# Performance work log

Hardware: AMD Instinct MI355X
Metric: run time of the kernel (lower is better)

Reference implementation:

```python
import jax, jax.numpy as jnp
import numpy as np

L1, L2, B = 512, 512, 2
D1, D2, BN = 256, 256, 256
NEG = jnp.float32(-1e12)


def setup_inputs() -> dict:
    key = jax.random.key(0)
    ks = jax.random.split(key, 8)
    s = 0.05
    return {
        "ctx_1": jax.random.normal(ks[0], (L1, B, D1), jnp.float32),
        "ctx_2": jax.random.normal(ks[1], (L2, B, D2), jnp.float32),
        "ctx_1_mask": jnp.ones((L1, B), jnp.float32),
        "ctx_2_mask": jnp.ones((L2, B), jnp.float32),
        # mlp_hid: Conv2d(D1+D2 -> BN, 1x1) with bias
        "Wh": jax.random.normal(ks[2], (D1 + D2, BN), jnp.float32) * s,
        "bh": jnp.zeros((BN,), jnp.float32),
        # mlp_out: Conv2d(BN -> 1, 1x1), bias=False (mlp_bias default)
        "wo": jax.random.normal(ks[3], (BN,), jnp.float32) * s,
        # project_1_to_2 / project_2_to_1: Linear(D1+D2 -> BN) with bias
        "W12": jax.random.normal(ks[4], (D2 + D1, BN), jnp.float32) * s,
        "b12": jnp.zeros((BN,), jnp.float32),
        "W21": jax.random.normal(ks[5], (D1 + D2, BN), jnp.float32) * s,
        "b21": jnp.zeros((BN,), jnp.float32),
    }


def reference(ctx_1, ctx_2, ctx_1_mask, ctx_2_mask, Wh, bh, wo, W12, b12, W21, b21):
    d1 = ctx_1.shape[-1]
    # 1x1 conv on cat([b_ctx_1, b_ctx_2]) == sum of two independent projections
    Wh1, Wh2 = Wh[:d1], Wh[d1:]
    p1 = jnp.einsum('lbd,dk->blk', ctx_1, Wh1)            # (B, L1, K)
    p2 = jnp.einsum('mbd,dk->bmk', ctx_2, Wh2)            # (B, L2, K)
    hidden = jnp.tanh(p1[:, :, None, :] + p2[:, None, :, :] + bh)  # (B, L1, L2, K)
    affinity = jnp.einsum('blmk,k->blm', hidden, wo)      # (B, L1, L2)
    # masked in both directions
    affinity = affinity + (1.0 - ctx_1_mask.T)[:, :, None] * NEG
    affinity = affinity + (1.0 - ctx_2_mask.T)[:, None, :] * NEG
    # 1 -> 2 direction: softmax over L2
    dist_1_to_2 = jax.nn.softmax(affinity, axis=2)        # (B, L1, L2)
    context_1_to_2 = jnp.einsum('lbd,blm->mbd', ctx_1, dist_1_to_2)  # (L2, B, D1)
    seq_1_to_2 = jnp.tanh(jnp.concatenate([ctx_2, context_1_to_2], axis=-1) @ W12 + b12)
    # 2 -> 1 direction: softmax over L1 (then contracted over L2, as in the torch code)
    dist_2_to_1 = jax.nn.softmax(affinity, axis=1)        # (B, L1, L2)
    context_2_to_1 = jnp.einsum('mbd,blm->lbd', ctx_2, dist_2_to_1)  # (L1, B, D2)
    seq_2_to_1 = jnp.tanh(jnp.concatenate([ctx_1, context_2_to_1], axis=-1) @ W21 + b21)
    return (seq_2_to_1, seq_1_to_2)
```

## Files before the change

kernel.cpp:

```cpp
#include <hip/hip_runtime.h>


#define NEGC (-1e12f)
#define TWO_LOG2E 2.8853900817779268f
#define LOG2E 1.4426950408889634f

typedef __attribute__((ext_vector_type(8))) short bf16x8;
typedef __attribute__((ext_vector_type(4))) float f32x4;

__device__ __forceinline__ short f2bf(float x)
{
    union { float f; unsigned u; } v; v.f = x;
    unsigned r = (v.u + 0x7FFFu + ((v.u >> 16) & 1u)) >> 16;
    return (short)r;
}

__global__ __launch_bounds__(256) void k_proj(
    const float* __restrict__ ctx1, const float* __restrict__ ctx2,
    const float* __restrict__ Wh, const float* __restrict__ bh,
    const float* __restrict__ W12, const float* __restrict__ b12,
    const float* __restrict__ W21, const float* __restrict__ b21,
    const float* __restrict__ mask1, const float* __restrict__ mask2,
    float* __restrict__ E1, float* __restrict__ E2,
    float* __restrict__ P12, float* __restrict__ U1,
    float* __restrict__ P21, float* __restrict__ U2,
    float* __restrict__ p1, float* __restrict__ p2,
    float* __restrict__ S1, float* __restrict__ S2)
{
    const int t  = threadIdx.x;
    const int g  = blockIdx.z;
    const int r0 = blockIdx.x * 64;
    const int n0 = blockIdx.y * 64;

    const float* A; const float* W; const float* bias; int expm; float* outp;
    switch (g) {
      case 0:  A=ctx1; W=Wh;        bias=bh;   expm=1; outp=E1;  break;
      case 1:  A=ctx2; W=Wh+65536;  bias=0;    expm=1; outp=E2;  break;
      case 2:  A=ctx2; W=W12;       bias=b12;  expm=0; outp=P12; break;
      case 3:  A=ctx1; W=W12+65536; bias=0;    expm=0; outp=U1;  break;
      case 4:  A=ctx1; W=W21;       bias=b21;  expm=0; outp=P21; break;
      default: A=ctx2; W=W21+65536; bias=0;    expm=0; outp=U2;  break;
    }

    if (g == 0 && blockIdx.x == 0 && blockIdx.y == 0) {
        for (int idx = t; idx < 1024; idx += 256) {
            int row = idx >> 1, b = idx & 1;
            p1[b * 512 + row] = __builtin_amdgcn_exp2f(LOG2E * (1.f - mask1[idx]) * NEGC);
            p2[b * 512 + row] = __builtin_amdgcn_exp2f(LOG2E * (1.f - mask2[idx]) * NEGC);
            S1[b * 512 + row] = 0.f;
            S2[b * 512 + row] = 0.f;
        }
    }

    __shared__ __align__(16) short Abf[64 * 136];
    __shared__ __align__(16) short Bbf[64 * 136];

    const int w    = t >> 6;
    const int lane = t & 63;
    const int quad = lane >> 4;
    const int lr   = lane & 15;

    f32x4 acc[4] = {};

    for (int kc = 0; kc < 256; kc += 128) {
        #pragma unroll
        for (int i = 0; i < 8; ++i) {
            int slot = i * 256 + t;
            int r = slot >> 5, kq = (slot & 31) << 2;
            float4 v = *(const float4*)(A + (r0 + r) * 256 + kc + kq);
            short4 s; s.x = f2bf(v.x); s.y = f2bf(v.y); s.z = f2bf(v.z); s.w = f2bf(v.w);
            *(short4*)(Abf + r * 136 + kq) = s;
        }
        #pragma unroll
        for (int i = 0; i < 8; ++i) {
            int slot = i * 256 + t;
            int bk = slot >> 4, bn4 = (slot & 15) << 2;
            float4 v = *(const float4*)(W + (kc + bk) * 256 + n0 + bn4);
            Bbf[(bn4 + 0) * 136 + bk] = f2bf(v.x);
            Bbf[(bn4 + 1) * 136 + bk] = f2bf(v.y);
            Bbf[(bn4 + 2) * 136 + bk] = f2bf(v.z);
            Bbf[(bn4 + 3) * 136 + bk] = f2bf(v.w);
        }
        __syncthreads();
        #pragma unroll
        for (int s = 0; s < 4; ++s) {
            const int kb = s * 32 + quad * 8;
            bf16x8 a = *(const bf16x8*)(Abf + (w * 16 + lr) * 136 + kb);
            #pragma unroll
            for (int nc = 0; nc < 4; ++nc) {
                bf16x8 b = *(const bf16x8*)(Bbf + (nc * 16 + lr) * 136 + kb);
                acc[nc] = __builtin_amdgcn_mfma_f32_16x16x32_bf16(a, b, acc[nc], 0, 0, 0);
            }
        }
        __syncthreads();
    }

    #pragma unroll
    for (int nc = 0; nc < 4; ++nc) {
        const int col = n0 + nc * 16 + lr;
        const float bv = bias ? bias[col] : 0.f;
        #pragma unroll
        for (int reg = 0; reg < 4; ++reg) {
            int row  = r0 + w * 16 + quad * 4 + reg;
            int orow = ((row & 1) << 9) + (row >> 1);
            float v = acc[nc][reg] + bv;
            if (expm) v = __builtin_amdgcn_exp2f(v * TWO_LOG2E);
            outp[orow * 256 + col] = v;
        }
    }
}

#define CELL2(AV, QV, ACC) do {                                       \
    float r0_ = __builtin_amdgcn_rcpf(fmaf(AV.x, QV.x, 1.f));         \
    float r1_ = __builtin_amdgcn_rcpf(fmaf(AV.y, QV.y, 1.f));         \
    float r2_ = __builtin_amdgcn_rcpf(fmaf(AV.z, QV.z, 1.f));         \
    float r3_ = __builtin_amdgcn_rcpf(fmaf(AV.w, QV.w, 1.f));         \
    ACC = fmaf(w.x, r0_, fmaf(w.y, r1_, fmaf(w.z, r2_,                \
          fmaf(w.w, r3_, ACC))));                                     \
} while (0)

__global__ __launch_bounds__(256) void k_aff(
    const float* __restrict__ E1g, const float* __restrict__ E2g,
    const float* __restrict__ wo,
    const float* __restrict__ p1g, const float* __restrict__ p2g,
    float* __restrict__ EN, float* __restrict__ ET,
    float* __restrict__ S1, float* __restrict__ S2)
{
    const int t  = threadIdx.x;
    const int l0 = blockIdx.x * 64, m0 = blockIdx.y * 32, b = blockIdx.z;

    __shared__ __align__(16) float E1s[64 * 132];
    __shared__ __align__(16) float E2s[32 * 132];
    __shared__ __align__(16) float affs[64 * 36];
    __shared__ __align__(16) float wos[256];

    wos[t] = -2.f * wo[t];
    const int tl = t >> 4, tm = t & 15;
    float acc[4][2] = {};

    for (int kc = 0; kc < 256; kc += 128) {
        #pragma unroll
        for (int i = 0; i < 8; ++i) {
            int slot = i * 256 + t;
            int r = slot >> 5, kq = (slot & 31) << 2;
            *(float4*)(E1s + r * 132 + kq) =
                *(const float4*)(E1g + (((b << 9) + l0 + r) << 8) + kc + kq);
        }
        #pragma unroll
        for (int i = 0; i < 4; ++i) {
            int slot = i * 256 + t;
            int r = slot >> 5, kq = (slot & 31) << 2;
            *(float4*)(E2s + r * 132 + kq) =
                *(const float4*)(E2g + (((b << 9) + m0 + r) << 8) + kc + kq);
        }
        __syncthreads();
        #pragma unroll 4
        for (int k0 = 0; k0 < 128; k0 += 4) {
            const float4 w  = *(const float4*)(wos + kc + k0);
            const float4 q0 = *(const float4*)(E2s + tm * 132 + k0);
            const float4 q1 = *(const float4*)(E2s + (tm + 16) * 132 + k0);
            #pragma unroll
            for (int i = 0; i < 4; ++i) {
                const float4 a = *(const float4*)(E1s + (tl + 16 * i) * 132 + k0);
                CELL2(a, q0, acc[i][0]);
                CELL2(a, q1, acc[i][1]);
            }
        }
        __syncthreads();
    }

    #pragma unroll
    for (int i = 0; i < 4; ++i) {
        affs[(tl + 16 * i) * 36 + tm]      = __builtin_amdgcn_exp2f(acc[i][0] * LOG2E);
        affs[(tl + 16 * i) * 36 + tm + 16] = __builtin_amdgcn_exp2f(acc[i][1] * LOG2E);
    }
    __syncthreads();

    #pragma unroll
    for (int i = 0; i < 2; ++i) {
        int slot = i * 256 + t;
        int r = slot >> 3, c4 = (slot & 7) << 2;
        float4 e   = *(const float4*)(affs + r * 36 + c4);
        const float p1r = p1g[(b << 9) + l0 + r];
        float4 vn = make_float4(e.x * p1r, e.y * p1r, e.z * p1r, e.w * p1r);
        *(float4*)(EN + (((b << 9) + l0 + r) << 9) + m0 + c4) = vn;
        float4 p2v = *(const float4*)(p2g + (b << 9) + m0 + c4);
        float s = (e.x * p2v.x + e.y * p2v.y) + (e.z * p2v.z + e.w * p2v.w);
        s += __shfl_xor(s, 1, 64);
        s += __shfl_xor(s, 2, 64);
        s += __shfl_xor(s, 4, 64);
        if ((t & 7) == 0) atomicAdd(S1 + (b << 9) + l0 + r, s);
    }
    #pragma unroll
    for (int i = 0; i < 2; ++i) {
        int slot = i * 256 + t;
        int r = slot >> 4, c4 = (slot & 15) << 2;
        float4 te;
        te.x = affs[(c4 + 0) * 36 + r];
        te.y = affs[(c4 + 1) * 36 + r];
        te.z = affs[(c4 + 2) * 36 + r];
        te.w = affs[(c4 + 3) * 36 + r];
        const float p2r = p2g[(b << 9) + m0 + r];
        float4 vt = make_float4(te.x * p2r, te.y * p2r, te.z * p2r, te.w * p2r);
        *(float4*)(ET + (((b << 9) + m0 + r) << 9) + l0 + c4) = vt;
        float4 p1v = *(const float4*)(p1g + (b << 9) + l0 + c4);
        float s = (te.x * p1v.x + te.y * p1v.y) + (te.z * p1v.z + te.w * p1v.w);
        s += __shfl_xor(s, 1, 64);
        s += __shfl_xor(s, 2, 64);
        s += __shfl_xor(s, 4, 64);
        s += __shfl_xor(s, 8, 64);
        if ((t & 15) == 0) atomicAdd(S2 + (b << 9) + m0 + r, s);
    }
}

__global__ __launch_bounds__(256) void k_final(
    const float* __restrict__ EN, const float* __restrict__ ET,
    const float* __restrict__ U1, const float* __restrict__ U2,
    const float* __restrict__ P12, const float* __restrict__ P21,
    const float* __restrict__ S1, const float* __restrict__ S2,
    float* __restrict__ out)
{
    const int t   = threadIdx.x;
    const int r0  = blockIdx.x * 32, n0 = blockIdx.y * 32;
    const int dir = blockIdx.z >> 1, b = blockIdx.z & 1;
    const float* Ag = (dir == 0 ? ET  : EN)  + b * 262144;
    const float* Sg = (dir == 0 ? S1  : S2)  + b * 512;
    const float* Bg = (dir == 0 ? U1  : U2)  + b * 131072;
    const float* Pg = (dir == 0 ? P12 : P21) + b * 131072;
    float* o = out + (dir == 0 ? 262144 : 0);

    __shared__ __align__(16) short Abf[32 * 72];
    __shared__ __align__(16) short Bbf[32 * 72];
    __shared__ __align__(16) float rs[512];

    for (int i = t; i < 512; i += 256)
        rs[i] = __builtin_amdgcn_rcpf(Sg[i]);
    __syncthreads();

    const int w    = t >> 6;
    const int lane = t & 63;
    const int quad = lane >> 4;
    const int lr   = lane & 15;
    const int wr   = (w >> 1) << 4, wc = (w & 1) << 4;
    f32x4 acc = {};

    for (int kc = 0; kc < 512; kc += 64) {
        #pragma unroll
        for (int i = 0; i < 2; ++i) {
            int slot = i * 256 + t;
            int r = slot >> 4, kq = (slot & 15) << 2;
            float4 v = *(const float4*)(Ag + ((r0 + r) << 9) + kc + kq);
            const float* rp = rs + kc + kq;
            short4 s;
            s.x = f2bf(v.x * rp[0]); s.y = f2bf(v.y * rp[1]);
            s.z = f2bf(v.z * rp[2]); s.w = f2bf(v.w * rp[3]);
            *(short4*)(Abf + r * 72 + kq) = s;
        }
        #pragma unroll
        for (int i = 0; i < 2; ++i) {
            int slot = i * 256 + t;
            int bk = slot >> 3, bn4 = (slot & 7) << 2;
            float4 v = *(const float4*)(Bg + ((kc + bk) << 8) + n0 + bn4);
            Bbf[(bn4 + 0) * 72 + bk] = f2bf(v.x);
            Bbf[(bn4 + 1) * 72 + bk] = f2bf(v.y);
            Bbf[(bn4 + 2) * 72 + bk] = f2bf(v.z);
            Bbf[(bn4 + 3) * 72 + bk] = f2bf(v.w);
        }
        __syncthreads();
        #pragma unroll
        for (int s = 0; s < 2; ++s) {
            const int kb = s * 32 + quad * 8;
            bf16x8 a = *(const bf16x8*)(Abf + (wr + lr) * 72 + kb);
            bf16x8 bb = *(const bf16x8*)(Bbf + (wc + lr) * 72 + kb);
            acc = __builtin_amdgcn_mfma_f32_16x16x32_bf16(a, bb, acc, 0, 0, 0);
        }
        __syncthreads();
    }

    const int col = n0 + wc + lr;
    #pragma unroll
    for (int reg = 0; reg < 4; ++reg) {
        const int m = r0 + wr + quad * 4 + reg;
        float v = acc[reg] + Pg[(m << 8) + col];
        float tv = 1.f - 2.f * __builtin_amdgcn_rcpf(
                       __builtin_amdgcn_exp2f(v * TWO_LOG2E) + 1.f);
        o[((m << 1) + b) * 256 + col] = tv;
    }
}

extern "C" void kernel_launch(void* const* d_in, const int* in_sizes, int n_in,
                              void* d_out, int out_size, void* d_ws, size_t ws_size,
                              hipStream_t stream)
{
    const float* ctx1 = (const float*)d_in[0];
    const float* ctx2 = (const float*)d_in[1];
    const float* m1   = (const float*)d_in[2];
    const float* m2   = (const float*)d_in[3];
    const float* Wh   = (const float*)d_in[4];
    const float* bh   = (const float*)d_in[5];
    const float* wo   = (const float*)d_in[6];
    const float* W12  = (const float*)d_in[7];
    const float* b12  = (const float*)d_in[8];
    const float* W21  = (const float*)d_in[9];
    const float* b21  = (const float*)d_in[10];
    float* out = (float*)d_out;
    float* ws  = (float*)d_ws;

    float* E1  = ws;
    float* E2  = E1  + 262144;
    float* P12 = E2  + 262144;
    float* U1  = P12 + 262144;
    float* P21 = U1  + 262144;
    float* U2  = P21 + 262144;
    float* p1  = U2  + 262144;
    float* p2  = p1  + 1024;
    float* S1  = p2  + 1024;
    float* S2  = S1  + 1024;
    float* EN  = S2  + 1024;
    float* ET  = EN  + 524288;

    hipLaunchKernelGGL(k_proj, dim3(16, 4, 6), dim3(256), 0, stream,
                       ctx1, ctx2, Wh, bh, W12, b12, W21, b21, m1, m2,
                       E1, E2, P12, U1, P21, U2, p1, p2, S1, S2);
    hipLaunchKernelGGL(k_aff, dim3(8, 16, 2), dim3(256), 0, stream,
                       E1, E2, wo, p1, p2, EN, ET, S1, S2);
    hipLaunchKernelGGL(k_final, dim3(16, 8, 4), dim3(256), 0, stream,
                       EN, ET, U1, U2, P12, P21, S1, S2, out);
}
```

Baseline: 120.8 us.

## Pair reciprocals in affinity loop and merge projection GEMMs sharing each input

The projection kernel now groups all three weight matrices that multiply the same input (ctx1 or ctx2) into one 768-wide GEMM. Each block computes a 64x96 tile, so each A tile is loaded and converted once per input instead of once per projection. In the affinity kernel, the four per-element reciprocals become two reciprocals of pairwise products with a weighted numerator, halving the transcendental count. The -2 scale on wo moves into the final exponent. The paired reciprocal risks overflow or precision loss when the products of (1+e1*e2) get large, and the 96-column tile adds per-element selection logic when loading weights.

After: 126.4 us. 4.6% more time.

```diff
diff --git a/kernel.cpp b/kernel.cpp
--- a/kernel.cpp
+++ b/kernel.cpp
@@ -4,6 +4,7 @@
 #define NEGC (-1e12f)
 #define TWO_LOG2E 2.8853900817779268f
 #define LOG2E 1.4426950408889634f
+#define N2LOG2E (-2.8853900817779268f)
 
 typedef __attribute__((ext_vector_type(8))) short bf16x8;
 typedef __attribute__((ext_vector_type(4))) float f32x4;
@@ -28,21 +29,13 @@
     float* __restrict__ S1, float* __restrict__ S2)
 {
     const int t  = threadIdx.x;
-    const int g  = blockIdx.z;
+    const int z  = blockIdx.z;
     const int r0 = blockIdx.x * 64;
-    const int n0 = blockIdx.y * 64;
-
-    const float* A; const float* W; const float* bias; int expm; float* outp;
-    switch (g) {
-      case 0:  A=ctx1; W=Wh;        bias=bh;   expm=1; outp=E1;  break;
-      case 1:  A=ctx2; W=Wh+65536;  bias=0;    expm=1; outp=E2;  break;
-      case 2:  A=ctx2; W=W12;       bias=b12;  expm=0; outp=P12; break;
-      case 3:  A=ctx1; W=W12+65536; bias=0;    expm=0; outp=U1;  break;
-      case 4:  A=ctx1; W=W21;       bias=b21;  expm=0; outp=P21; break;
-      default: A=ctx2; W=W21+65536; bias=0;    expm=0; outp=U2;  break;
-    }
-
-    if (g == 0 && blockIdx.x == 0 && blockIdx.y == 0) {
+    const int n0 = blockIdx.y * 96;
+
+    const float* A = z ? ctx2 : ctx1;
+
+    if (z == 0 && blockIdx.x == 0 && blockIdx.y == 0) {
         for (int idx = t; idx < 1024; idx += 256) {
             int row = idx >> 1, b = idx & 1;
             p1[b * 512 + row] = __builtin_amdgcn_exp2f(LOG2E * (1.f - mask1[idx]) * NEGC);
@@ -53,14 +46,14 @@
     }
 
     __shared__ __align__(16) short Abf[64 * 136];
-    __shared__ __align__(16) short Bbf[64 * 136];
+    __shared__ __align__(16) short Bbf[96 * 136];
 
     const int w    = t >> 6;
     const int lane = t & 63;
     const int quad = lane >> 4;
     const int lr   = lane & 15;
 
-    f32x4 acc[4] = {};
+    f32x4 acc[6] = {};
 
     for (int kc = 0; kc < 256; kc += 128) {
         #pragma unroll
@@ -72,10 +65,18 @@
             *(short4*)(Abf + r * 136 + kq) = s;
         }
         #pragma unroll
-        for (int i = 0; i < 8; ++i) {
-            int slot = i * 256 + t;
-            int bk = slot >> 4, bn4 = (slot & 15) << 2;
-            float4 v = *(const float4*)(W + (kc + bk) * 256 + n0 + bn4);
+        for (int i = 0; i < 12; ++i) {
+            int slot = i * 256 + t;
+            int bk = slot / 24;
+            int bn4 = (slot - bk * 24) << 2;
+            int ncol = n0 + bn4;
+            int gsel = ncol >> 8;
+            int c = ncol & 255;
+            const float* Wp; int rbase;
+            if (gsel == 0)      { Wp = Wh;  rbase = z ? 256 : 0; }
+            else if (gsel == 1) { Wp = W12; rbase = z ? 0 : 256; }
+            else                { Wp = W21; rbase = z ? 256 : 0; }
+            float4 v = *(const float4*)(Wp + (rbase + kc + bk) * 256 + c);
             Bbf[(bn4 + 0) * 136 + bk] = f2bf(v.x);
             Bbf[(bn4 + 1) * 136 + bk] = f2bf(v.y);
             Bbf[(bn4 + 2) * 136 + bk] = f2bf(v.z);
@@ -87,7 +88,7 @@
             const int kb = s * 32 + quad * 8;
             bf16x8 a = *(const bf16x8*)(Abf + (w * 16 + lr) * 136 + kb);
             #pragma unroll
-            for (int nc = 0; nc < 4; ++nc) {
+            for (int nc = 0; nc < 6; ++nc) {
                 bf16x8 b = *(const bf16x8*)(Bbf + (nc * 16 + lr) * 136 + kb);
                 acc[nc] = __builtin_amdgcn_mfma_f32_16x16x32_bf16(a, b, acc[nc], 0, 0, 0);
             }
@@ -96,8 +97,20 @@
     }
 
     #pragma unroll
-    for (int nc = 0; nc < 4; ++nc) {
-        const int col = n0 + nc * 16 + lr;
+    for (int nc = 0; nc < 6; ++nc) {
+        const int ncb  = n0 + nc * 16;
+        const int gsel = ncb >> 8;
+        const int col  = (ncb & 255) + lr;
+        float* outp; const float* bias; int expm;
+        if (z == 0) {
+            if (gsel == 0)      { outp = E1;  bias = bh;      expm = 1; }
+            else if (gsel == 1) { outp = U1;  bias = nullptr; expm = 0; }
+            else                { outp = P21; bias = b21;     expm = 0; }
+        } else {
+            if (gsel == 0)      { outp = E2;  bias = nullptr; expm = 1; }
+            else if (gsel == 1) { outp = P12; bias = b12;     expm = 0; }
+            else                { outp = U2;  bias = nullptr; expm = 0; }
+        }
         const float bv = bias ? bias[col] : 0.f;
         #pragma unroll
         for (int reg = 0; reg < 4; ++reg) {
@@ -110,13 +123,17 @@
     }
 }
 
-#define CELL2(AV, QV, ACC) do {                                       \
-    float r0_ = __builtin_amdgcn_rcpf(fmaf(AV.x, QV.x, 1.f));         \
-    float r1_ = __builtin_amdgcn_rcpf(fmaf(AV.y, QV.y, 1.f));         \
-    float r2_ = __builtin_amdgcn_rcpf(fmaf(AV.z, QV.z, 1.f));         \
-    float r3_ = __builtin_amdgcn_rcpf(fmaf(AV.w, QV.w, 1.f));         \
-    ACC = fmaf(w.x, r0_, fmaf(w.y, r1_, fmaf(w.z, r2_,                \
-          fmaf(w.w, r3_, ACC))));                                     \
+#define PAIR(AV, QV, WV, ACC) do {                                    \
+    float x0_ = fmaf(AV.x, QV.x, 1.f);                                \
+    float x1_ = fmaf(AV.y, QV.y, 1.f);                                \
+    float x2_ = fmaf(AV.z, QV.z, 1.f);                                \
+    float x3_ = fmaf(AV.w, QV.w, 1.f);                                \
+    float r01_ = __builtin_amdgcn_rcpf(x0_ * x1_);                    \
+    float r23_ = __builtin_amdgcn_rcpf(x2_ * x3_);                    \
+    float z01_ = fmaf(WV.y, x0_, WV.x * x1_);                         \
+    float z23_ = fmaf(WV.w, x2_, WV.z * x3_);                         \
+    ACC = fmaf(r01_, z01_, ACC);                                      \
+    ACC = fmaf(r23_, z23_, ACC);                                      \
 } while (0)
 
 __global__ __launch_bounds__(256) void k_aff(
@@ -132,9 +149,7 @@
     __shared__ __align__(16) float E1s[64 * 132];
     __shared__ __align__(16) float E2s[32 * 132];
     __shared__ __align__(16) float affs[64 * 36];
-    __shared__ __align__(16) float wos[256];
-
-    wos[t] = -2.f * wo[t];
+
     const int tl = t >> 4, tm = t & 15;
     float acc[4][2] = {};
 
@@ -156,14 +171,14 @@
         __syncthreads();
         #pragma unroll 4
         for (int k0 = 0; k0 < 128; k0 += 4) {
-            const float4 w  = *(const float4*)(wos + kc + k0);
+            const float4 w  = *(const float4*)(wo + kc + k0);
             const float4 q0 = *(const float4*)(E2s + tm * 132 + k0);
             const float4 q1 = *(const float4*)(E2s + (tm + 16) * 132 + k0);
             #pragma unroll
             for (int i = 0; i < 4; ++i) {
                 const float4 a = *(const float4*)(E1s + (tl + 16 * i) * 132 + k0);
-                CELL2(a, q0, acc[i][0]);
-                CELL2(a, q1, acc[i][1]);
+                PAIR(a, q0, w, acc[i][0]);
+                PAIR(a, q1, w, acc[i][1]);
             }
         }
         __syncthreads();
@@ -171,8 +186,8 @@
 
     #pragma unroll
     for (int i = 0; i < 4; ++i) {
-        affs[(tl + 16 * i) * 36 + tm]      = __builtin_amdgcn_exp2f(acc[i][0] * LOG2E);
-        affs[(tl + 16 * i) * 36 + tm + 16] = __builtin_amdgcn_exp2f(acc[i][1] * LOG2E);
+        affs[(tl + 16 * i) * 36 + tm]      = __builtin_amdgcn_exp2f(acc[i][0] * N2LOG2E);
+        affs[(tl + 16 * i) * 36 + tm + 16] = __builtin_amdgcn_exp2f(acc[i][1] * N2LOG2E);
     }
     __syncthreads();
 
@@ -319,7 +334,7 @@
     float* EN  = S2  + 1024;
     float* ET  = EN  + 524288;
 
-    hipLaunchKernelGGL(k_proj, dim3(16, 4, 6), dim3(256), 0, stream,
+    hipLaunchKernelGGL(k_proj, dim3(16, 8, 2), dim3(256), 0, stream,
                        ctx1, ctx2, Wh, bh, W12, b12, W21, b21, m1, m2,
                        E1, E2, P12, U1, P21, U2, p1, p2, S1, S2);
     hipLaunchKernelGGL(k_aff, dim3(8, 16, 2), dim3(256), 0, stream,
```

## Pair reciprocals in affinity kernel and shrink tile to 32x32

Applied to the files above, without the earlier changes.

Combines two reciprocal terms into one by computing w0/x0 + w1/x1 as (w1*x0 + w0*x1)/(x0*x1), which halves the number of rcp instructions in the tanh-based affinity inner loop. The -2 scale on wo moves into the final exp constant, so the shared wo buffer goes away and wo is read straight from global memory. The l tile also shrinks from 64 to 32 rows, doubling the block count to improve occupancy at the cost of less reuse per block. Multiplying x0*x1 can overflow or lose precision when inputs are large.

Result: no change. 118.8 us (-1.7%).

```diff
diff --git a/kernel.cpp b/kernel.cpp
--- a/kernel.cpp
+++ b/kernel.cpp
@@ -4,6 +4,7 @@
 #define NEGC (-1e12f)
 #define TWO_LOG2E 2.8853900817779268f
 #define LOG2E 1.4426950408889634f
+#define N2LOG2E (-2.8853900817779268f)
 
 typedef __attribute__((ext_vector_type(8))) short bf16x8;
 typedef __attribute__((ext_vector_type(4))) float f32x4;
@@ -110,13 +111,17 @@
     }
 }
 
-#define CELL2(AV, QV, ACC) do {                                       \
-    float r0_ = __builtin_amdgcn_rcpf(fmaf(AV.x, QV.x, 1.f));         \
-    float r1_ = __builtin_amdgcn_rcpf(fmaf(AV.y, QV.y, 1.f));         \
-    float r2_ = __builtin_amdgcn_rcpf(fmaf(AV.z, QV.z, 1.f));         \
-    float r3_ = __builtin_amdgcn_rcpf(fmaf(AV.w, QV.w, 1.f));         \
-    ACC = fmaf(w.x, r0_, fmaf(w.y, r1_, fmaf(w.z, r2_,                \
-          fmaf(w.w, r3_, ACC))));                                     \
+#define PAIR(AV, QV, WV, ACC) do {                                    \
+    float x0_ = fmaf(AV.x, QV.x, 1.f);                                \
+    float x1_ = fmaf(AV.y, QV.y, 1.f);                                \
+    float x2_ = fmaf(AV.z, QV.z, 1.f);                                \
+    float x3_ = fmaf(AV.w, QV.w, 1.f);                                \
+    float r01_ = __builtin_amdgcn_rcpf(x0_ * x1_);                    \
+    float r23_ = __builtin_amdgcn_rcpf(x2_ * x3_);                    \
+    float z01_ = fmaf(WV.y, x0_, WV.x * x1_);                         \
+    float z23_ = fmaf(WV.w, x2_, WV.z * x3_);                         \
+    ACC = fmaf(r01_, z01_, ACC);                                      \
+    ACC = fmaf(r23_, z23_, ACC);                                      \
 } while (0)
 
 __global__ __launch_bounds__(256) void k_aff(
@@ -127,60 +132,51 @@
     float* __restrict__ S1, float* __restrict__ S2)
 {
     const int t  = threadIdx.x;
-    const int l0 = blockIdx.x * 64, m0 = blockIdx.y * 32, b = blockIdx.z;
-
-    __shared__ __align__(16) float E1s[64 * 132];
+    const int l0 = blockIdx.x * 32, m0 = blockIdx.y * 32, b = blockIdx.z;
+
+    __shared__ __align__(16) float E1s[32 * 132];
     __shared__ __align__(16) float E2s[32 * 132];
-    __shared__ __align__(16) float affs[64 * 36];
-    __shared__ __align__(16) float wos[256];
-
-    wos[t] = -2.f * wo[t];
+    __shared__ __align__(16) float affs[32 * 36];
+
     const int tl = t >> 4, tm = t & 15;
-    float acc[4][2] = {};
+    float acc[2][2] = {};
 
     for (int kc = 0; kc < 256; kc += 128) {
         #pragma unroll
-        for (int i = 0; i < 8; ++i) {
+        for (int i = 0; i < 4; ++i) {
             int slot = i * 256 + t;
             int r = slot >> 5, kq = (slot & 31) << 2;
             *(float4*)(E1s + r * 132 + kq) =
                 *(const float4*)(E1g + (((b << 9) + l0 + r) << 8) + kc + kq);
-        }
-        #pragma unroll
-        for (int i = 0; i < 4; ++i) {
-            int slot = i * 256 + t;
-            int r = slot >> 5, kq = (slot & 31) << 2;
             *(float4*)(E2s + r * 132 + kq) =
                 *(const float4*)(E2g + (((b << 9) + m0 + r) << 8) + kc + kq);
         }
         __syncthreads();
         #pragma unroll 4
         for (int k0 = 0; k0 < 128; k0 += 4) {
-            const float4 w  = *(const float4*)(wos + kc + k0);
+            const float4 w  = *(const float4*)(wo + kc + k0);
+            const float4 a0 = *(const float4*)(E1s + tl * 132 + k0);
+            const float4 a1 = *(const float4*)(E1s + (tl + 16) * 132 + k0);
             const float4 q0 = *(const float4*)(E2s + tm * 132 + k0);
             const float4 q1 = *(const float4*)(E2s + (tm + 16) * 132 + k0);
-            #pragma unroll
-            for (int i = 0; i < 4; ++i) {
-                const float4 a = *(const float4*)(E1s + (tl + 16 * i) * 132 + k0);
-                CELL2(a, q0, acc[i][0]);
-                CELL2(a, q1, acc[i][1]);
-            }
-        }
-        __syncthreads();
-    }
-
-    #pragma unroll
-    for (int i = 0; i < 4; ++i) {
-        affs[(tl + 16 * i) * 36 + tm]      = __builtin_amdgcn_exp2f(acc[i][0] * LOG2E);
-        affs[(tl + 16 * i) * 36 + tm + 16] = __builtin_amdgcn_exp2f(acc[i][1] * LOG2E);
-    }
+            PAIR(a0, q0, w, acc[0][0]);
+            PAIR(a0, q1, w, acc[0][1]);
+            PAIR(a1, q0, w, acc[1][0]);
+            PAIR(a1, q1, w, acc[1][1]);
+        }
+        __syncthreads();
+    }
+
+    affs[tl * 36 + tm]             = __builtin_amdgcn_exp2f(acc[0][0] * N2LOG2E);
+    affs[tl * 36 + tm + 16]        = __builtin_amdgcn_exp2f(acc[0][1] * N2LOG2E);
+    affs[(tl + 16) * 36 + tm]      = __builtin_amdgcn_exp2f(acc[1][0] * N2LOG2E);
+    affs[(tl + 16) * 36 + tm + 16] = __builtin_amdgcn_exp2f(acc[1][1] * N2LOG2E);
     __syncthreads();
 
-    #pragma unroll
-    for (int i = 0; i < 2; ++i) {
-        int slot = i * 256 + t;
-        int r = slot >> 3, c4 = (slot & 7) << 2;
-        float4 e   = *(const float4*)(affs + r * 36 + c4);
+    const int r  = t >> 3;
+    const int c4 = (t & 7) << 2;
+    {
+        float4 e = *(const float4*)(affs + r * 36 + c4);
         const float p1r = p1g[(b << 9) + l0 + r];
         float4 vn = make_float4(e.x * p1r, e.y * p1r, e.z * p1r, e.w * p1r);
         *(float4*)(EN + (((b << 9) + l0 + r) << 9) + m0 + c4) = vn;
@@ -191,10 +187,7 @@
         s += __shfl_xor(s, 4, 64);
         if ((t & 7) == 0) atomicAdd(S1 + (b << 9) + l0 + r, s);
     }
-    #pragma unroll
-    for (int i = 0; i < 2; ++i) {
-        int slot = i * 256 + t;
-        int r = slot >> 4, c4 = (slot & 15) << 2;
+    {
         float4 te;
         te.x = affs[(c4 + 0) * 36 + r];
         te.y = affs[(c4 + 1) * 36 + r];
@@ -208,8 +201,7 @@
         s += __shfl_xor(s, 1, 64);
         s += __shfl_xor(s, 2, 64);
         s += __shfl_xor(s, 4, 64);
-        s += __shfl_xor(s, 8, 64);
-        if ((t & 15) == 0) atomicAdd(S2 + (b << 9) + m0 + r, s);
+        if ((t & 7) == 0) atomicAdd(S2 + (b << 9) + m0 + r, s);
     }
 }
 
@@ -322,7 +314,7 @@
     hipLaunchKernelGGL(k_proj, dim3(16, 4, 6), dim3(256), 0, stream,
                        ctx1, ctx2, Wh, bh, W12, b12, W21, b21, m1, m2,
                        E1, E2, P12, U1, P21, U2, p1, p2, S1, S2);
-    hipLaunchKernelGGL(k_aff, dim3(8, 16, 2), dim3(256), 0, stream,
+    hipLaunchKernelGGL(k_aff, dim3(16, 16, 2), dim3(256), 0, stream,
                        E1, E2, wo, p1, p2, EN, ET, S1, S2);
     hipLaunchKernelGGL(k_final, dim3(16, 8, 4), dim3(256), 0, stream,
                        EN, ET, U1, U2, P12, P21, S1, S2, out);
```
